# Performance work log

Measured on AMD Instinct MI355X. Metric: run time of the kernel, lower is better.

The kernel has to match this reference:

```python
import jax, jax.numpy as jnp
import numpy as np

B, C_IN, H, W = 4, 128, 56, 56
G = 4            # num_groups
K = 3            # kernel_size
PAD = 1
STRIDE = 1
NG = 8           # grid_size (num RBF centers)
GRID_MIN, GRID_MAX = -1.0, 1.0
C_OUT = 128
CG = C_IN // G           # 32 channels per group
D = CG * K * K           # 288 per-group patch dim
OG = C_OUT // G          # 32 outputs per group


def setup_inputs() -> dict:
    key = jax.random.key(0)
    k1, k2, k3, k4 = jax.random.split(key, 4)
    x = jax.random.normal(k1, (B, C_IN, H, W), dtype=jnp.float32)
    spline_w = jax.random.normal(k2, (G, OG, D * NG), dtype=jnp.float32) * (1.0 / np.sqrt(D * NG))
    base_w = jax.random.normal(k3, (G, OG, D), dtype=jnp.float32) * (1.0 / np.sqrt(D))
    base_b = jax.random.normal(k4, (G, OG), dtype=jnp.float32) * 0.01
    return {"x": x, "spline_w": spline_w, "base_w": base_w, "base_b": base_b}


def _im2col(x):
    # x: (B, C, H, W) -> patches (B, C*K*K, Ho, Wo), unfold ordering (c, kh, kw)
    xp = jnp.pad(x, ((0, 0), (0, 0), (PAD, PAD), (PAD, PAD)))
    Ho = (H + 2 * PAD - K) // STRIDE + 1
    Wo = (W + 2 * PAD - K) // STRIDE + 1
    # fixed 3x3 loop over kernel offsets (9 slices), vectorized over B,C,H,W
    shards = [xp[:, :, i:i + Ho, j:j + Wo] for i in range(K) for j in range(K)]
    p = jnp.stack(shards, axis=2)             # (B, C, K*K, Ho, Wo)
    return p.reshape(x.shape[0], -1, Ho, Wo)  # (B, C*K*K, Ho, Wo)


def reference(x, spline_w, base_w, base_b):
    Ho = (H + 2 * PAD - K) // STRIDE + 1
    Wo = (W + 2 * PAD - K) // STRIDE + 1
    L = Ho * Wo
    patches = _im2col(x)                                   # (B, C*9, Ho, Wo)
    # groups are contiguous channel blocks -> split channel-major patch dim
    p = patches.reshape(B, G, D, L).transpose(0, 1, 3, 2)  # (B, G, L, D)
    # RBF spline basis: exp(-((x - c)/h)^2)
    grid = jnp.linspace(GRID_MIN, GRID_MAX, NG, dtype=p.dtype)   # (NG,)
    h = (GRID_MAX - GRID_MIN) / (NG - 1)
    basis = jnp.exp(-(((p[..., None] - grid) / h) ** 2))         # (B, G, L, D, NG)
    basis = basis.reshape(B, G, L, D * NG)
    spline_out = jnp.einsum('bgld,god->bglo', basis, spline_w)   # (B, G, L, OG)
    base_out = jnp.einsum('bgld,god->bglo', jax.nn.silu(p), base_w) + base_b[None, :, None, :]
    out = spline_out + base_out                                  # (B, G, L, OG)
    # torch.cat(group outs, dim=1) -> per-pixel channel order is group-major
    out = out.transpose(0, 2, 1, 3).reshape(B, L, G * OG)        # (B, L, C_OUT)
    out = out.transpose(0, 2, 1).reshape(B, C_OUT, Ho, Wo)
    return out
```

## Files before the change

kernel.cpp:

```cpp
#include <hip/hip_runtime.h>

#define BATCH 4
#define C_IN 128
#define HWD 56
#define L_PIX 3136
#define G_GRP 4
#define CG 32
#define D_DIM 288
#define NG 8
#define OG 32
#define NQ_SPL 72
#define NQ_BASE 9
#define LOG2E 1.44269504f
#define SQRT_L 1.2011224087f
#define A_SCL  4.2039284306f

typedef short  short8 __attribute__((ext_vector_type(8)));
typedef float  f32x4  __attribute__((ext_vector_type(4)));
typedef unsigned int u32x4 __attribute__((ext_vector_type(4)));

__device__ __forceinline__ unsigned int pack2(float lo, float hi) {
    unsigned short a = __builtin_bit_cast(unsigned short, (__bf16)lo);
    unsigned short b = __builtin_bit_cast(unsigned short, (__bf16)hi);
    return (unsigned int)a | ((unsigned int)b << 16);
}

#define N_SPL_CHUNK (G_GRP * OG * D_DIM)
#define N_BASE_CHUNK (G_GRP * OG * D_DIM / 8)

__global__ __launch_bounds__(256) void convert_w_kernel(
    const float* __restrict__ spline_w,
    const float* __restrict__ base_w,
    short* __restrict__ wspl,
    short* __restrict__ wbase)
{
    int t = blockIdx.x * 256 + threadIdx.x;
    if (t >= N_SPL_CHUNK + N_BASE_CHUNK) return;
    if (t < N_SPL_CHUNK) {
        const f32x4* s4 = (const f32x4*)spline_w + (size_t)t * 2;
        f32x4 lo = s4[0], hi = s4[1];
        int flat = t * 8;
        int g = flat / (OG * D_DIM * NG);
        int r = flat - g * (OG * D_DIM * NG);
        int o = r / (D_DIM * NG);
        int d = (r - o * (D_DIM * NG)) >> 3;
        int dl = d / 72;
        int q  = d - dl * 72;
        int lane = dl * 16 + (o & 15);
        int ot = o >> 4;
        u32x4 pk;
        pk.x = pack2(lo.x, lo.y); pk.y = pack2(lo.z, lo.w);
        pk.z = pack2(hi.x, hi.y); pk.w = pack2(hi.z, hi.w);
        u32x4* dst = (u32x4*)wspl + (((size_t)(g * NQ_SPL + q) * 2 + ot) * 64 + lane);
        *dst = pk;
    } else {
        int tb = t - N_SPL_CHUNK;
        const f32x4* s4 = (const f32x4*)base_w + (size_t)tb * 2;
        f32x4 lo = s4[0], hi = s4[1];
        int flat = tb * 8;
        int g = flat / (OG * D_DIM);
        int r = flat - g * (OG * D_DIM);
        int o = r / D_DIM;
        int d0 = r - o * D_DIM;
        int dl = d0 / 72;
        int q  = (d0 - dl * 72) >> 3;
        int lane = dl * 16 + (o & 15);
        int ot = o >> 4;
        u32x4 pk;
        pk.x = pack2(lo.x, lo.y); pk.y = pack2(lo.z, lo.w);
        pk.z = pack2(hi.x, hi.y); pk.w = pack2(hi.z, hi.w);
        u32x4* dst = (u32x4*)wbase + (((size_t)(g * NQ_BASE + q) * 2 + ot) * 64 + lane);
        *dst = pk;
    }
}

__global__ __launch_bounds__(256, 3) void groupkan_mfma_kernel(
    const float* __restrict__ x,
    const float* __restrict__ base_b,
    const short* __restrict__ wspl,
    const short* __restrict__ wbase,
    float* __restrict__ out)
{
    __shared__ float xt[CG][4][58];

    const int tid  = threadIdx.x;
    const int tile = blockIdx.x;
    const int bg   = blockIdx.y;
    const int b = bg >> 2, g = bg & 3;
    const int l0 = tile * 64;
    const int y0 = l0 / HWD;

    const float* xg = x + (size_t)(b * C_IN + g * CG) * L_PIX;
    for (int e = tid; e < CG * 4 * 58; e += 256) {
        int c  = e / 232;
        int r  = e - c * 232;
        int ry = r / 58;
        int rx = r - ry * 58;
        int y  = y0 - 1 + ry;
        int xc = rx - 1;
        float v = 0.0f;
        if (y >= 0 && y < HWD && xc >= 0 && xc < HWD)
            v = xg[(size_t)c * L_PIX + y * HWD + xc];
        xt[c][ry][rx] = v;
    }
    __syncthreads();

    const int lane = tid & 63;
    const int wid  = tid >> 6;
    const int fr   = lane & 15;
    const int dl   = lane >> 4;
    const int l    = l0 + wid * 16 + fr;
    const int yy   = l / HWD;
    const int xx   = l - yy * HWD;
    const int ybase = yy - y0;

    const float* P = (const float*)xt + (dl * 8) * 232 + ybase * 58 + xx;

    f32x4 acc0, acc1;
    {
        float b0 = base_b[g * OG + fr];
        float b1 = base_b[g * OG + 16 + fr];
        acc0 = (f32x4){b0, b0, b0, b0};
        acc1 = (f32x4){b1, b1, b1, b1};
    }

    const short8* wl  = (const short8*)wspl + (size_t)g * NQ_SPL * 2 * 64 + lane;
    const short8* wbl = (const short8*)wbase + (size_t)g * NQ_BASE * 2 * 64 + lane;

    for (int qo = 0; qo < 8; ++qo) {
        const float* Pc = P + qo * 232;
#pragma unroll
        for (int qi = 0; qi < 9; ++qi) {
            const int kh = qi / 3, kw = qi % 3;
            float v  = Pc[kh * 58 + kw];
            float ap = v * A_SCL + A_SCL;
            float e0, e1, e2, e3, e4, e5, e6, e7;
            {
                float u;
                u = ap - 0.0f * SQRT_L; e0 = __builtin_amdgcn_exp2f(-(u * u));
                u = ap - 1.0f * SQRT_L; e1 = __builtin_amdgcn_exp2f(-(u * u));
                u = ap - 2.0f * SQRT_L; e2 = __builtin_amdgcn_exp2f(-(u * u));
                u = ap - 3.0f * SQRT_L; e3 = __builtin_amdgcn_exp2f(-(u * u));
                u = ap - 4.0f * SQRT_L; e4 = __builtin_amdgcn_exp2f(-(u * u));
                u = ap - 5.0f * SQRT_L; e5 = __builtin_amdgcn_exp2f(-(u * u));
                u = ap - 6.0f * SQRT_L; e6 = __builtin_amdgcn_exp2f(-(u * u));
                u = ap - 7.0f * SQRT_L; e7 = __builtin_amdgcn_exp2f(-(u * u));
            }
            u32x4 pk;
            pk.x = pack2(e0, e1); pk.y = pack2(e2, e3);
            pk.z = pack2(e4, e5); pk.w = pack2(e6, e7);
            short8 a = __builtin_bit_cast(short8, pk);
            const int q = qo * 9 + qi;
            short8 bf0 = wl[(q * 2 + 0) * 64];
            short8 bf1 = wl[(q * 2 + 1) * 64];
            acc0 = __builtin_amdgcn_mfma_f32_16x16x32_bf16(a, bf0, acc0, 0, 0, 0);
            acc1 = __builtin_amdgcn_mfma_f32_16x16x32_bf16(a, bf1, acc1, 0, 0, 0);
        }
    }

#pragma unroll
    for (int q = 0; q < 9; ++q) {
        float s0, s1, s2, s3, s4, s5, s6, s7;
#pragma unroll
        for (int j = 0; j < 8; ++j) {
            const int dd = 8 * q + j;
            const int co = dd / 9, kk = dd % 9;
            const int kh = kk / 3, kw = kk % 3;
            float v  = P[co * 232 + kh * 58 + kw];
            float ex = __builtin_amdgcn_exp2f(-(v * LOG2E));
            float s  = v * __builtin_amdgcn_rcpf(1.0f + ex);
            if (j == 0) s0 = s; else if (j == 1) s1 = s; else if (j == 2) s2 = s;
            else if (j == 3) s3 = s; else if (j == 4) s4 = s; else if (j == 5) s5 = s;
            else if (j == 6) s6 = s; else s7 = s;
        }
        u32x4 pk;
        pk.x = pack2(s0, s1); pk.y = pack2(s2, s3);
        pk.z = pack2(s4, s5); pk.w = pack2(s6, s7);
        short8 a = __builtin_bit_cast(short8, pk);
        short8 bf0 = wbl[(q * 2 + 0) * 64];
        short8 bf1 = wbl[(q * 2 + 1) * 64];
        acc0 = __builtin_amdgcn_mfma_f32_16x16x32_bf16(a, bf0, acc0, 0, 0, 0);
        acc1 = __builtin_amdgcn_mfma_f32_16x16x32_bf16(a, bf1, acc1, 0, 0, 0);
    }

    float* outp = out + (size_t)(b * C_IN + g * OG) * L_PIX;
    int pix = l0 + wid * 16 + dl * 4;
    *(f32x4*)(outp + (size_t)fr * L_PIX + pix)        = acc0;
    *(f32x4*)(outp + (size_t)(16 + fr) * L_PIX + pix) = acc1;
}

extern "C" void kernel_launch(void* const* d_in, const int* in_sizes, int n_in,
                              void* d_out, int out_size, void* d_ws, size_t ws_size,
                              hipStream_t stream) {
    const float* x        = (const float*)d_in[0];
    const float* spline_w = (const float*)d_in[1];
    const float* base_w   = (const float*)d_in[2];
    const float* base_b   = (const float*)d_in[3];
    float* out = (float*)d_out;

    short* wspl  = (short*)d_ws;
    short* wbase = wspl + (size_t)G_GRP * NQ_SPL * 2 * 64 * 8;

    int conv_threads = N_SPL_CHUNK + N_BASE_CHUNK;
    convert_w_kernel<<<(conv_threads + 255) / 256, 256, 0, stream>>>(
        spline_w, base_w, wspl, wbase);

    dim3 grid(L_PIX / 64, BATCH * G_GRP);
    groupkan_mfma_kernel<<<grid, 256, 0, stream>>>(x, base_b, wspl, wbase, out);
}
```

Baseline: 110.7 us.

## Compute RBF basis via exp recurrence and pad LDS channel stride

Replaces the eight independent exp2 evaluations per input value with two exp2 calls plus a multiplicative recurrence. It uses symmetry (flipping about the grid midpoint) so the recurrence runs from the nearest end, and clamps each term to 1. Separately, the shared-memory tile's per-channel stride is padded from 232 to 233 floats to reduce LDS bank conflicts between lanes reading different channels. The recurrence trades transcendental throughput for a dependent multiply chain with selects, which adds some accuracy risk in bf16.

```diff
diff --git a/kernel.cpp b/kernel.cpp
--- a/kernel.cpp
+++ b/kernel.cpp
@@ -11,9 +11,9 @@
 #define OG 32
 #define NQ_SPL 72
 #define NQ_BASE 9
-#define LOG2E 1.44269504f
-#define SQRT_L 1.2011224087f
-#define A_SCL  4.2039284306f
+#define L2E 1.44269504f
+#define TWO_L2E 2.88539008f
+#define XSTRIDE 233
 
 typedef short  short8 __attribute__((ext_vector_type(8)));
 typedef float  f32x4  __attribute__((ext_vector_type(4)));
@@ -81,7 +81,7 @@
     const short* __restrict__ wbase,
     float* __restrict__ out)
 {
-    __shared__ float xt[CG][4][58];
+    __shared__ float xt[CG * XSTRIDE];
 
     const int tid  = threadIdx.x;
     const int tile = blockIdx.x;
@@ -91,7 +91,7 @@
     const int y0 = l0 / HWD;
 
     const float* xg = x + (size_t)(b * C_IN + g * CG) * L_PIX;
-    for (int e = tid; e < CG * 4 * 58; e += 256) {
+    for (int e = tid; e < CG * 232; e += 256) {
         int c  = e / 232;
         int r  = e - c * 232;
         int ry = r / 58;
@@ -101,7 +101,7 @@
         float v = 0.0f;
         if (y >= 0 && y < HWD && xc >= 0 && xc < HWD)
             v = xg[(size_t)c * L_PIX + y * HWD + xc];
-        xt[c][ry][rx] = v;
+        xt[c * XSTRIDE + r] = v;
     }
     __syncthreads();
 
@@ -114,7 +114,7 @@
     const int xx   = l - yy * HWD;
     const int ybase = yy - y0;
 
-    const float* P = (const float*)xt + (dl * 8) * 232 + ybase * 58 + xx;
+    const float* P = xt + (dl * 8) * XSTRIDE + ybase * 58 + xx;
 
     f32x4 acc0, acc1;
     {
@@ -128,33 +128,41 @@
     const short8* wbl = (const short8*)wbase + (size_t)g * NQ_BASE * 2 * 64 + lane;
 
     for (int qo = 0; qo < 8; ++qo) {
-        const float* Pc = P + qo * 232;
+        const float* Pc = P + qo * XSTRIDE;
 #pragma unroll
         for (int qi = 0; qi < 9; ++qi) {
             const int kh = qi / 3, kw = qi % 3;
             float v  = Pc[kh * 58 + kw];
-            float ap = v * A_SCL + A_SCL;
-            float e0, e1, e2, e3, e4, e5, e6, e7;
-            {
-                float u;
-                u = ap - 0.0f * SQRT_L; e0 = __builtin_amdgcn_exp2f(-(u * u));
-                u = ap - 1.0f * SQRT_L; e1 = __builtin_amdgcn_exp2f(-(u * u));
-                u = ap - 2.0f * SQRT_L; e2 = __builtin_amdgcn_exp2f(-(u * u));
-                u = ap - 3.0f * SQRT_L; e3 = __builtin_amdgcn_exp2f(-(u * u));
-                u = ap - 4.0f * SQRT_L; e4 = __builtin_amdgcn_exp2f(-(u * u));
-                u = ap - 5.0f * SQRT_L; e5 = __builtin_amdgcn_exp2f(-(u * u));
-                u = ap - 6.0f * SQRT_L; e6 = __builtin_amdgcn_exp2f(-(u * u));
-                u = ap - 7.0f * SQRT_L; e7 = __builtin_amdgcn_exp2f(-(u * u));
-            }
+            float a  = __builtin_fmaf(v, 3.5f, 3.5f);
+            bool flip = a > 3.5f;
+            float aa = flip ? 7.0f - a : a;
+            float t  = (aa * L2E) * aa;
+            float f0 = __builtin_amdgcn_exp2f(-t);
+            float R  = __builtin_amdgcn_exp2f(aa * TWO_L2E);
+            float f1 = fminf((f0 * R) * 0.36787944f,   1.0f);
+            float f2 = fminf((f1 * R) * 0.049787068f,  1.0f);
+            float f3 = fminf((f2 * R) * 6.7379470e-3f, 1.0f);
+            float f4 = fminf((f3 * R) * 9.1188197e-4f, 1.0f);
+            float f5 = fminf((f4 * R) * 1.2340980e-4f, 1.0f);
+            float f6 = fminf((f5 * R) * 1.6701700e-5f, 1.0f);
+            float f7 = fminf((f6 * R) * 2.2603294e-6f, 1.0f);
+            float e0 = flip ? f7 : f0;
+            float e1 = flip ? f6 : f1;
+            float e2 = flip ? f5 : f2;
+            float e3 = flip ? f4 : f3;
+            float e4 = flip ? f3 : f4;
+            float e5 = flip ? f2 : f5;
+            float e6 = flip ? f1 : f6;
+            float e7 = flip ? f0 : f7;
             u32x4 pk;
             pk.x = pack2(e0, e1); pk.y = pack2(e2, e3);
             pk.z = pack2(e4, e5); pk.w = pack2(e6, e7);
-            short8 a = __builtin_bit_cast(short8, pk);
+            short8 aF = __builtin_bit_cast(short8, pk);
             const int q = qo * 9 + qi;
             short8 bf0 = wl[(q * 2 + 0) * 64];
             short8 bf1 = wl[(q * 2 + 1) * 64];
-            acc0 = __builtin_amdgcn_mfma_f32_16x16x32_bf16(a, bf0, acc0, 0, 0, 0);
-            acc1 = __builtin_amdgcn_mfma_f32_16x16x32_bf16(a, bf1, acc1, 0, 0, 0);
+            acc0 = __builtin_amdgcn_mfma_f32_16x16x32_bf16(aF, bf0, acc0, 0, 0, 0);
+            acc1 = __builtin_amdgcn_mfma_f32_16x16x32_bf16(aF, bf1, acc1, 0, 0, 0);
         }
     }
 
@@ -166,8 +174,8 @@
             const int dd = 8 * q + j;
             const int co = dd / 9, kk = dd % 9;
             const int kh = kk / 3, kw = kk % 3;
-            float v  = P[co * 232 + kh * 58 + kw];
-            float ex = __builtin_amdgcn_exp2f(-(v * LOG2E));
+            float v  = P[co * XSTRIDE + kh * 58 + kw];
+            float ex = __builtin_amdgcn_exp2f(-(v * L2E));
             float s  = v * __builtin_amdgcn_rcpf(1.0f + ex);
             if (j == 0) s0 = s; else if (j == 1) s1 = s; else if (j == 2) s2 = s;
             else if (j == 3) s3 = s; else if (j == 4) s4 = s; else if (j == 5) s5 = s;
@@ -176,11 +184,11 @@
         u32x4 pk;
         pk.x = pack2(s0, s1); pk.y = pack2(s2, s3);
         pk.z = pack2(s4, s5); pk.w = pack2(s6, s7);
-        short8 a = __builtin_bit_cast(short8, pk);
+        short8 aF = __builtin_bit_cast(short8, pk);
         short8 bf0 = wbl[(q * 2 + 0) * 64];
         short8 bf1 = wbl[(q * 2 + 1) * 64];
-        acc0 = __builtin_amdgcn_mfma_f32_16x16x32_bf16(a, bf0, acc0, 0, 0, 0);
-        acc1 = __builtin_amdgcn_mfma_f32_16x16x32_bf16(a, bf1, acc1, 0, 0, 0);
+        acc0 = __builtin_amdgcn_mfma_f32_16x16x32_bf16(aF, bf0, acc0, 0, 0, 0);
+        acc1 = __builtin_amdgcn_mfma_f32_16x16x32_bf16(aF, bf1, acc1, 0, 0, 0);
     }
 
     float* outp = out + (size_t)(b * C_IN + g * OG) * L_PIX;
```

Result: no change. 112.5 us (+1.6%).
